# Kernel optimization log

Hardware: AMD Instinct MI355X
Metric: run time of the kernel (lower is better)

Reference implementation:

```python
import jax, jax.numpy as jnp
import numpy as np
import math

HGT, WID = 24, 24          # shape2d
NUM_HEADS = 12
EMB = 768
HEAD_DIM = EMB // NUM_HEADS
N_GRID = HGT * WID         # 576 spatial tokens
N_TOK = N_GRID + 1         # +1 CLS token
BATCH = 32


def _rel_indices(h: int, w: int) -> np.ndarray:
    """[(h*w), (h*w)] indices into the (2h-1)*(2w-1) relative table."""
    y = np.arange(h)
    x = np.arange(w)
    y1, x1, y2, x2 = np.meshgrid(y, x, y, x, indexing='ij')
    idx = (y1 - y2 + h - 1) * (2 * w - 1) + (x1 - x2 + w - 1)
    return idx.reshape(h * w, h * w)


def setup_inputs() -> dict:
    key = jax.random.key(0)
    ks = jax.random.split(key, 6)
    s = 0.02
    return {
        "x": jax.random.normal(ks[0], (BATCH, N_TOK, EMB), dtype=jnp.float32),
        "Wq": jax.random.normal(ks[1], (EMB, EMB), dtype=jnp.float32) * s,
        "bq": jnp.zeros((EMB,), dtype=jnp.float32),
        "Wk": jax.random.normal(ks[2], (EMB, EMB), dtype=jnp.float32) * s,
        "bk": jnp.zeros((EMB,), dtype=jnp.float32),
        "Wv": jax.random.normal(ks[3], (EMB, EMB), dtype=jnp.float32) * s,
        "bv": jnp.zeros((EMB,), dtype=jnp.float32),
        "Wp": jax.random.normal(ks[4], (EMB, EMB), dtype=jnp.float32) * s,
        "bp": jnp.zeros((EMB,), dtype=jnp.float32),
        "rel_table": jax.random.normal(ks[5], ((2 * HGT - 1) * (2 * WID - 1), NUM_HEADS), dtype=jnp.float32) * s,
    }


def reference(x, Wq, bq, Wk, bk, Wv, bv, Wp, bp, rel_table):
    B, N, E = x.shape
    scale = 1.0 / math.sqrt(HEAD_DIM)

    def heads(t):  # [B,N,E] -> [B,H,N,hd]
        return t.reshape(B, N, NUM_HEADS, HEAD_DIM).transpose(0, 2, 1, 3)

    q = heads(x @ Wq.T + bq)
    k = heads(x @ Wk.T + bk)
    v = heads(x @ Wv.T + bv)

    scores = jnp.einsum('bhqd,bhkd->bhqk', q, k) * scale  # [B,H,N,N]

    # relative position bias on spatial tokens (skip CLS row/col)
    idx = jnp.asarray(_rel_indices(HGT, WID))              # [Ng,Ng]
    bias = rel_table[idx].transpose(2, 0, 1)               # [H,Ng,Ng]
    scores = scores.at[:, :, 1:, 1:].add(bias)

    attn = jax.nn.softmax(scores, axis=-1)
    out = jnp.einsum('bhqk,bhkd->bhqd', attn, v)           # [B,H,N,hd]
    out = out.transpose(0, 2, 1, 3).reshape(B, N, E)
    return out @ Wp.T + bp
```

## Files before the change

kernel.cpp:

```cpp
#include <hip/hip_runtime.h>
#include <stdint.h>

#define HGT   24
#define WID   24
#define NHEAD 12
#define EMB   768
#define HD    64
#define NGRID 576
#define NTOK  577
#define NPAD  640
#define BATCH 32
#define MROWS (BATCH * NTOK)
#define NKT   10
#define NQT   5
#define QKVC  (3 * EMB)

typedef __attribute__((ext_vector_type(8))) short bf16x8;
typedef __attribute__((ext_vector_type(4))) float f32x4;

__device__ __forceinline__ short f2bf(float f) {
    union { float f; unsigned u; } c; c.f = f;
    unsigned r = (c.u + 0x7FFFu + ((c.u >> 16) & 1u)) >> 16;
    return (short)(r & 0xFFFFu);
}
__device__ __forceinline__ float b2f(short s) {
    union { unsigned u; float f; } c; c.u = ((unsigned)(unsigned short)s) << 16;
    return c.f;
}

__device__ __forceinline__ void gload16(void* lds, const void* g) {
    __builtin_amdgcn_global_load_lds(
        (const __attribute__((address_space(1))) void*)g,
        (__attribute__((address_space(3))) void*)lds, 16, 0, 0);
}

__device__ __forceinline__ void wait_vm0_barrier() {
    asm volatile("s_waitcnt vmcnt(0)" ::: "memory");
    __builtin_amdgcn_s_barrier();
}

__device__ __forceinline__ int xcd_swizzle(int orig, int nwg) {
    int q = nwg >> 3, r = nwg & 7;
    int xcd = orig & 7, idx = orig >> 3;
    return (xcd < r) ? xcd * (q + 1) + idx : r * (q + 1) + (xcd - r) * q + idx;
}

__global__ void cast_f32_bf16(const float* __restrict__ src, short* __restrict__ dst, int n) {
    int i = (blockIdx.x * blockDim.x + threadIdx.x) * 4;
    int stride = gridDim.x * blockDim.x * 4;
    for (int j = i; j < n; j += stride) {
        float4 v = *(const float4*)(src + j);
        short4 o;
        o.x = f2bf(v.x); o.y = f2bf(v.y); o.z = f2bf(v.z); o.w = f2bf(v.w);
        *(short4*)(dst + j) = o;
    }
}

__global__ void bias_expand(const float* __restrict__ rel, short* __restrict__ be) {
    int q = blockIdx.x;
    int k = threadIdx.x;
    float v[NHEAD];
    if (k >= NTOK) {
#pragma unroll
        for (int h = 0; h < NHEAD; h++) v[h] = -1e30f;
    } else if (q == 0 || q >= NTOK || k == 0) {
#pragma unroll
        for (int h = 0; h < NHEAD; h++) v[h] = 0.f;
    } else {
        int i = q - 1, j = k - 1;
        int idx = ((i / WID) - (j / WID) + HGT - 1) * (2 * WID - 1)
                + ((i % WID) - (j % WID) + WID - 1);
        const float* rp = rel + (size_t)idx * NHEAD;
#pragma unroll
        for (int h = 0; h < NHEAD; h++) v[h] = rp[h];
    }
#pragma unroll
    for (int h = 0; h < NHEAD; h++)
        be[((size_t)h * NPAD + q) * NPAD + k] = f2bf(v[h]);
}

__global__ __launch_bounds__(256) void transpose_v(const short* __restrict__ qnat, short* __restrict__ vt) {
    __shared__ __align__(16) short T[64][72];
    int bi = blockIdx.x;
    int kt = bi % NKT;
    int h  = (bi / NKT) % NHEAD;
    int b  = bi / (NKT * NHEAD);
    int t  = threadIdx.x;

    int r  = t >> 2, cb = (t & 3) * 16;
    int key = kt * 64 + r; if (key >= NTOK) key = NTOK - 1;
    const short* src = qnat + (size_t)(b * NTOK + key) * QKVC + 2 * EMB + h * HD;
    *(int4*)&T[r][cb]     = *(const int4*)(src + cb);
    *(int4*)&T[r][cb + 8] = *(const int4*)(src + cb + 8);
    __syncthreads();

    int d = t >> 2, kb = (t & 3) * 16;
    short tmp[16];
#pragma unroll
    for (int s = 0; s < 16; s++) tmp[s] = T[kb + s][d];
    short* dst = vt + (((size_t)b * NHEAD + h) * HD + d) * NPAD + kt * 64 + kb;
    *(int4*)&dst[0] = *(int4*)&tmp[0];
    *(int4*)&dst[8] = *(int4*)&tmp[8];
}

template <int MODE>
__global__ __launch_bounds__(256) void gemm_bt(
    const short* __restrict__ A, const short* __restrict__ Bw,
    const float* __restrict__ b0, const float* __restrict__ b1, const float* __restrict__ b2,
    void* __restrict__ Outp, int M)
{
    constexpr int NC  = (MODE == 0) ? QKVC : EMB;
    constexpr int NBX = NC / 128;
    constexpr int K   = EMB;
    constexpr int NST = K / 128;

    __shared__ __align__(16) short Asl[128][128];
    __shared__ __align__(16) short Bsl[128][128];

    const int t    = threadIdx.x;
    const int lane = t & 63;
    const int w    = t >> 6;
    const int wr   = (w >> 1) * 64;
    const int wc   = (w & 1) * 64;
    const int lg   = lane >> 4;
    const int li   = lane & 15;

    const int nwg  = NBX * 145;
    const int wgid = xcd_swizzle(blockIdx.x, nwg);
    const int tm   = (wgid / NBX) * 128;
    const int tn   = (wgid % NBX) * 128;

    const int srow16 = w * 4 + (lane >> 4);
    const int cofs   = ((lane & 15) ^ srow16) * 8;

    const short* ag[8];
    const short* bg[8];
#pragma unroll
    for (int p = 0; p < 8; p++) {
        int rm = tm + p * 16 + srow16; if (rm >= M) rm = M - 1;
        ag[p] = A  + (size_t)rm * K + cofs;
        bg[p] = Bw + (size_t)(tn + p * 16 + srow16) * K + cofs;
    }

    f32x4 acc[4][4];
#pragma unroll
    for (int i = 0; i < 4; i++)
#pragma unroll
        for (int j = 0; j < 4; j++) acc[i][j] = (f32x4){0.f, 0.f, 0.f, 0.f};

#pragma unroll
    for (int p = 0; p < 8; p++) {
        gload16(&Asl[p * 16 + w * 4][0], ag[p]);
        gload16(&Bsl[p * 16 + w * 4][0], bg[p]);
    }

    for (int step = 0; step < NST; step++) {
        wait_vm0_barrier();

#pragma unroll
        for (int kk = 0; kk < 4; kk++) {
            bf16x8 af[4], bfr[4];
#pragma unroll
            for (int i = 0; i < 4; i++)
                af[i]  = *(const bf16x8*)&Asl[wr + i * 16 + li][((kk * 4 + lg) ^ li) * 8];
#pragma unroll
            for (int j = 0; j < 4; j++)
                bfr[j] = *(const bf16x8*)&Bsl[wc + j * 16 + li][((kk * 4 + lg) ^ li) * 8];
#pragma unroll
            for (int i = 0; i < 4; i++)
#pragma unroll
                for (int j = 0; j < 4; j++)
                    acc[i][j] = __builtin_amdgcn_mfma_f32_16x16x32_bf16(af[i], bfr[j], acc[i][j], 0, 0, 0);
        }

        __builtin_amdgcn_s_barrier();
        if (step + 1 < NST) {
            int k0 = (step + 1) * 128;
#pragma unroll
            for (int p = 0; p < 8; p++) {
                gload16(&Asl[p * 16 + w * 4][0], ag[p] + k0);
                gload16(&Bsl[p * 16 + w * 4][0], bg[p] + k0);
            }
        }
    }

#pragma unroll
    for (int j = 0; j < 4; j++) {
        int c = tn + wc + j * 16 + li;
        float bias;
        if constexpr (MODE == 0) {
            int which = (c >= 2 * EMB) ? 2 : ((c >= EMB) ? 1 : 0);
            const float* bb = (which == 0) ? b0 : ((which == 1) ? b1 : b2);
            bias = bb[c - which * EMB];
        } else {
            bias = b0[c];
        }
#pragma unroll
        for (int i = 0; i < 4; i++) {
#pragma unroll
            for (int r = 0; r < 4; r++) {
                int m = tm + wr + i * 16 + lg * 4 + r;
                if (m >= M) continue;
                float v = acc[i][j][r] + bias;
                if constexpr (MODE == 0)
                    ((short*)Outp)[(size_t)m * NC + c] = f2bf(v);
                else
                    ((float*)Outp)[(size_t)m * NC + c] = v;
            }
        }
    }
}

__global__ __launch_bounds__(512) void attn_kernel(
    const short* __restrict__ qnat, const short* __restrict__ vt,
    const short* __restrict__ biasx, short* __restrict__ aout)
{
    __shared__ __align__(16) short Ksl[2][64][64];
    __shared__ __align__(16) short Vsl[2][64][64];
    __shared__ __align__(16) short Psl[8][16][72];

    const int wg = (blockIdx.x & 7) * (BATCH * NHEAD * NQT / 8) + (blockIdx.x >> 3);
    const int qt = wg % NQT;
    const int rest = wg / NQT;
    const int b  = rest & 31;
    const int h  = rest >> 5;

    const int t    = threadIdx.x;
    const int lane = t & 63;
    const int w    = t >> 6;
    const int lg   = lane >> 4;
    const int li   = lane & 15;
    const int xh   = li & 7;
    const int qbase = qt * 128;
    const int myq  = qbase + w * 16 + li;

    const short* qp  = qnat + (size_t)b * NTOK * QKVC + h * HD;
    const short* kp  = qp + EMB;
    const short* vtp = vt + ((size_t)b * NHEAD + h) * (size_t)HD * NPAD;
    const short* browq = biasx + ((size_t)h * NPAD + myq) * NPAD;

    bf16x8 qf[2];
    {
        int qrow = myq < NTOK ? myq : NTOK - 1;
        qf[0] = *(const bf16x8*)(qp + (size_t)qrow * QKVC + lg * 8);
        qf[1] = *(const bf16x8*)(qp + (size_t)qrow * QKVC + 32 + lg * 8);
    }

    float mrun = -1e30f, lrun = 0.f;
    f32x4 oacc[4];
#pragma unroll
    for (int d = 0; d < 4; d++) oacc[d] = (f32x4){0.f, 0.f, 0.f, 0.f};

    const int srow = w * 8 + (lane >> 3);
    const int cofs = ((lane & 7) ^ (lane >> 3)) * 8;

    {
        int key = srow; if (key >= NTOK) key = NTOK - 1;
        gload16(&Ksl[0][w * 8][0], kp + (size_t)key * QKVC + cofs);
        gload16(&Vsl[0][w * 8][0], vtp + (size_t)srow * NPAD + cofs);
    }
    wait_vm0_barrier();

    short (*Kc)[64] = Ksl[0], (*Kn)[64] = Ksl[1];
    short (*Vc)[64] = Vsl[0], (*Vn)[64] = Vsl[1];

    for (int kt = 0; kt < NKT; kt++) {
        if (kt + 1 < NKT) {
            int key = (kt + 1) * 64 + srow; if (key >= NTOK) key = NTOK - 1;
            gload16(&Kn[w * 8][0], kp + (size_t)key * QKVC + cofs);
            gload16(&Vn[w * 8][0], vtp + (size_t)srow * NPAD + (kt + 1) * 64 + cofs);
        }

        float pvv[4][4];
        __builtin_amdgcn_s_setprio(1);
#pragma unroll
        for (int j = 0; j < 4; j++) {
            short4 bs = *(const short4*)&browq[kt * 64 + j * 16 + lg * 4];
            bf16x8 ak0 = *(const bf16x8*)&Kc[j * 16 + li][(lg ^ xh) * 8];
            bf16x8 ak1 = *(const bf16x8*)&Kc[j * 16 + li][((4 + lg) ^ xh) * 8];
            f32x4 s = (f32x4){0.f, 0.f, 0.f, 0.f};
            s = __builtin_amdgcn_mfma_f32_16x16x32_bf16(ak0, qf[0], s, 0, 0, 0);
            s = __builtin_amdgcn_mfma_f32_16x16x32_bf16(ak1, qf[1], s, 0, 0, 0);
            pvv[j][0] = fmaf(s[0], 0.125f, b2f(bs.x));
            pvv[j][1] = fmaf(s[1], 0.125f, b2f(bs.y));
            pvv[j][2] = fmaf(s[2], 0.125f, b2f(bs.z));
            pvv[j][3] = fmaf(s[3], 0.125f, b2f(bs.w));
        }
        __builtin_amdgcn_s_setprio(0);

        float mt = pvv[0][0];
#pragma unroll
        for (int j = 0; j < 4; j++)
#pragma unroll
            for (int r = 0; r < 4; r++) mt = fmaxf(mt, pvv[j][r]);
        mt = fmaxf(mt, __shfl_xor(mt, 16, 64));
        mt = fmaxf(mt, __shfl_xor(mt, 32, 64));
        float nm  = fmaxf(mrun, mt);
        float fac = __expf(mrun - nm);
        float rs  = 0.f;
#pragma unroll
        for (int j = 0; j < 4; j++)
#pragma unroll
            for (int r = 0; r < 4; r++) {
                float p = __expf(pvv[j][r] - nm);
                pvv[j][r] = p;
                rs += p;
            }
        rs += __shfl_xor(rs, 16, 64);
        rs += __shfl_xor(rs, 32, 64);
        lrun = lrun * fac + rs;
        mrun = nm;
#pragma unroll
        for (int d = 0; d < 4; d++) oacc[d] *= fac;

#pragma unroll
        for (int j = 0; j < 4; j++) {
            short4 ps;
            ps.x = f2bf(pvv[j][0]); ps.y = f2bf(pvv[j][1]);
            ps.z = f2bf(pvv[j][2]); ps.w = f2bf(pvv[j][3]);
            *(short4*)&Psl[w][li][j * 16 + lg * 4] = ps;
        }

        __builtin_amdgcn_s_setprio(1);
#pragma unroll
        for (int dd = 0; dd < 4; dd++) {
#pragma unroll
            for (int kk = 0; kk < 2; kk++) {
                bf16x8 av = *(const bf16x8*)&Vc[dd * 16 + li][((kk * 4 + lg) ^ xh) * 8];
                bf16x8 pb = *(const bf16x8*)&Psl[w][li][kk * 32 + lg * 8];
                oacc[dd] = __builtin_amdgcn_mfma_f32_16x16x32_bf16(av, pb, oacc[dd], 0, 0, 0);
            }
        }
        __builtin_amdgcn_s_setprio(0);

        wait_vm0_barrier();
        short (*tp)[64];
        tp = Kc; Kc = Kn; Kn = tp;
        tp = Vc; Vc = Vn; Vn = tp;
    }

    if (myq < NTOK) {
        float inv = 1.0f / lrun;
        short* op = aout + ((size_t)b * NTOK + myq) * EMB + h * HD;
#pragma unroll
        for (int dd = 0; dd < 4; dd++) {
            short4 o;
            o.x = f2bf(oacc[dd][0] * inv);
            o.y = f2bf(oacc[dd][1] * inv);
            o.z = f2bf(oacc[dd][2] * inv);
            o.w = f2bf(oacc[dd][3] * inv);
            *(short4*)&op[dd * 16 + lg * 4] = o;
        }
    }
}

extern "C" void kernel_launch(void* const* d_in, const int* in_sizes, int n_in,
                              void* d_out, int out_size, void* d_ws, size_t ws_size,
                              hipStream_t stream) {
    (void)in_sizes; (void)n_in; (void)out_size; (void)ws_size;
    const float* x   = (const float*)d_in[0];
    const float* Wq  = (const float*)d_in[1];
    const float* bq  = (const float*)d_in[2];
    const float* Wk  = (const float*)d_in[3];
    const float* bk  = (const float*)d_in[4];
    const float* Wv  = (const float*)d_in[5];
    const float* bv  = (const float*)d_in[6];
    const float* Wp  = (const float*)d_in[7];
    const float* bp  = (const float*)d_in[8];
    const float* rel = (const float*)d_in[9];

    const size_t WN = (size_t)EMB * EMB;
    short* Wb   = (short*)d_ws;
    short* Wpb  = Wb + 3 * WN;
    short* qnat = Wpb + WN;
    short* xb   = qnat + (size_t)MROWS * QKVC;
    short* aout = xb;
    short* vtb  = xb + (size_t)MROWS * EMB;
    short* bexp = vtb + (size_t)BATCH * NHEAD * HD * NPAD;

    const int XN = MROWS * EMB;
    cast_f32_bf16<<<576, 256, 0, stream>>>(Wq, Wb, (int)WN);
    cast_f32_bf16<<<576, 256, 0, stream>>>(Wk, Wb + WN, (int)WN);
    cast_f32_bf16<<<576, 256, 0, stream>>>(Wv, Wb + 2 * WN, (int)WN);
    cast_f32_bf16<<<576, 256, 0, stream>>>(Wp, Wpb, (int)WN);
    cast_f32_bf16<<<13848, 256, 0, stream>>>(x, xb, XN);
    bias_expand<<<NPAD, NPAD, 0, stream>>>(rel, bexp);

    gemm_bt<0><<<18 * 145, 256, 0, stream>>>(xb, Wb, bq, bk, bv, qnat, MROWS);
    transpose_v<<<BATCH * NHEAD * NKT, 256, 0, stream>>>(qnat, vtb);
    attn_kernel<<<BATCH * NHEAD * NQT, 512, 0, stream>>>(qnat, vtb, bexp, aout);
    gemm_bt<1><<<6 * 145, 256, 0, stream>>>(aout, Wpb, bp, bp, bp, d_out, MROWS);
}
```

Before: 315.7 us.

## Restructure GEMM to 256x256 tiles with double-buffered LDS and interleaved prefetch

The shared bf16 GEMM now uses 256x256 output tiles per 512-thread workgroup with a K-step of 64. The LDS is double-buffered, and the next tile's global loads are spread across the four compute sub-phases, with partial vmcnt waits and barriers between them. MFMA sections are wrapped in s_setprio to favour the math waves. The goal is to hide global-load latency and raise per-workgroup data reuse. The costs are fewer workgroups (9*73 and 3*73), higher register pressure from 32 accumulators per wave, and more barriers per K-step.

```diff
diff --git a/kernel.cpp b/kernel.cpp
--- a/kernel.cpp
+++ b/kernel.cpp
@@ -104,108 +104,148 @@
 }
 
 template <int MODE>
-__global__ __launch_bounds__(256) void gemm_bt(
+__global__ __launch_bounds__(512) void gemm_bt(
     const short* __restrict__ A, const short* __restrict__ Bw,
     const float* __restrict__ b0, const float* __restrict__ b1, const float* __restrict__ b2,
     void* __restrict__ Outp, int M)
 {
     constexpr int NC  = (MODE == 0) ? QKVC : EMB;
-    constexpr int NBX = NC / 128;
+    constexpr int NBX = NC / 256;
     constexpr int K   = EMB;
-    constexpr int NST = K / 128;
-
-    __shared__ __align__(16) short Asl[128][128];
-    __shared__ __align__(16) short Bsl[128][128];
+    constexpr int NT  = K / 64;
+
+    __shared__ __align__(16) short Asl[2][256][64];
+    __shared__ __align__(16) short Bsl[2][256][64];
 
     const int t    = threadIdx.x;
     const int lane = t & 63;
     const int w    = t >> 6;
-    const int wr   = (w >> 1) * 64;
-    const int wc   = (w & 1) * 64;
+    const int wm   = w >> 2;
+    const int wn   = w & 3;
     const int lg   = lane >> 4;
     const int li   = lane & 15;
-
-    const int nwg  = NBX * 145;
+    const int xh   = li & 7;
+
+    const int nwg  = NBX * ((MROWS + 255) / 256);
     const int wgid = xcd_swizzle(blockIdx.x, nwg);
-    const int tm   = (wgid / NBX) * 128;
-    const int tn   = (wgid % NBX) * 128;
-
-    const int srow16 = w * 4 + (lane >> 4);
-    const int cofs   = ((lane & 15) ^ srow16) * 8;
-
-    const short* ag[8];
-    const short* bg[8];
-#pragma unroll
-    for (int p = 0; p < 8; p++) {
-        int rm = tm + p * 16 + srow16; if (rm >= M) rm = M - 1;
-        ag[p] = A  + (size_t)rm * K + cofs;
-        bg[p] = Bw + (size_t)(tn + p * 16 + srow16) * K + cofs;
-    }
-
-    f32x4 acc[4][4];
-#pragma unroll
-    for (int i = 0; i < 4; i++)
+    const int tm   = (wgid / NBX) * 256;
+    const int tn   = (wgid % NBX) * 256;
+
+    const int srow = w * 8 + (lane >> 3);
+    const int cofs = ((lane & 7) ^ (lane >> 3)) * 8;
+
+    constexpr int AOFF[4] = {0, 128, 64, 192};
+    constexpr int BOFF[4] = {0, 64, 128, 192};
+
+    const short* agp[4];
+    const short* bgp[4];
+#pragma unroll
+    for (int i = 0; i < 4; i++) {
+        int ra = tm + AOFF[i] + srow; if (ra >= M) ra = M - 1;
+        agp[i] = A  + (size_t)ra * K + cofs;
+        bgp[i] = Bw + (size_t)(tn + BOFF[i] + srow) * K + cofs;
+    }
+
+    f32x4 acc[8][4];
+#pragma unroll
+    for (int i = 0; i < 8; i++)
 #pragma unroll
         for (int j = 0; j < 4; j++) acc[i][j] = (f32x4){0.f, 0.f, 0.f, 0.f};
 
 #pragma unroll
-    for (int p = 0; p < 8; p++) {
-        gload16(&Asl[p * 16 + w * 4][0], ag[p]);
-        gload16(&Bsl[p * 16 + w * 4][0], bg[p]);
-    }
-
-    for (int step = 0; step < NST; step++) {
-        wait_vm0_barrier();
-
-#pragma unroll
-        for (int kk = 0; kk < 4; kk++) {
-            bf16x8 af[4], bfr[4];
-#pragma unroll
-            for (int i = 0; i < 4; i++)
-                af[i]  = *(const bf16x8*)&Asl[wr + i * 16 + li][((kk * 4 + lg) ^ li) * 8];
-#pragma unroll
-            for (int j = 0; j < 4; j++)
-                bfr[j] = *(const bf16x8*)&Bsl[wc + j * 16 + li][((kk * 4 + lg) ^ li) * 8];
-#pragma unroll
-            for (int i = 0; i < 4; i++)
-#pragma unroll
-                for (int j = 0; j < 4; j++)
-                    acc[i][j] = __builtin_amdgcn_mfma_f32_16x16x32_bf16(af[i], bfr[j], acc[i][j], 0, 0, 0);
-        }
-
-        __builtin_amdgcn_s_barrier();
-        if (step + 1 < NST) {
-            int k0 = (step + 1) * 128;
-#pragma unroll
-            for (int p = 0; p < 8; p++) {
-                gload16(&Asl[p * 16 + w * 4][0], ag[p] + k0);
-                gload16(&Bsl[p * 16 + w * 4][0], bg[p] + k0);
+    for (int i = 0; i < 4; i++) gload16(&Bsl[0][BOFF[i] + w * 8][0], bgp[i]);
+#pragma unroll
+    for (int i = 0; i < 4; i++) gload16(&Asl[0][AOFF[i] + w * 8][0], agp[i]);
+    asm volatile("s_waitcnt vmcnt(2)" ::: "memory");
+    __builtin_amdgcn_s_barrier();
+
+    for (int kt = 0; kt < NT; kt++) {
+        const int c = kt & 1, nb = c ^ 1;
+        const bool more = (kt + 1 < NT);
+        const int k0n = (kt + 1) * 64;
+
+        bf16x8 bf[4][2];
+#pragma unroll
+        for (int q = 0; q < 4; q++) {
+            bf16x8 af[2][2];
+#pragma unroll
+            for (int mm = 0; mm < 2; mm++)
+#pragma unroll
+                for (int kk = 0; kk < 2; kk++)
+                    af[mm][kk] = *(const bf16x8*)
+                        &Asl[c][wm * 128 + (q * 2 + mm) * 16 + li][((kk * 4 + lg) ^ xh) * 8];
+            if (q == 0) {
+#pragma unroll
+                for (int nj = 0; nj < 4; nj++)
+#pragma unroll
+                    for (int kk = 0; kk < 2; kk++)
+                        bf[nj][kk] = *(const bf16x8*)
+                            &Bsl[c][wn * 64 + nj * 16 + li][((kk * 4 + lg) ^ xh) * 8];
             }
-        }
-    }
-
-#pragma unroll
-    for (int j = 0; j < 4; j++) {
-        int c = tn + wc + j * 16 + li;
+
+            if (q == 0) {
+                if (more) {
+                    gload16(&Bsl[nb][BOFF[0] + w * 8][0], bgp[0] + k0n);
+                    gload16(&Bsl[nb][BOFF[1] + w * 8][0], bgp[1] + k0n);
+                }
+            } else if (q == 1) {
+                if (more) {
+                    gload16(&Bsl[nb][BOFF[2] + w * 8][0], bgp[2] + k0n);
+                    gload16(&Bsl[nb][BOFF[3] + w * 8][0], bgp[3] + k0n);
+                    asm volatile("s_waitcnt vmcnt(4)" ::: "memory");
+                } else {
+                    asm volatile("s_waitcnt vmcnt(0)" ::: "memory");
+                }
+            } else if (q == 2) {
+                if (more) {
+                    gload16(&Asl[nb][AOFF[0] + w * 8][0], agp[0] + k0n);
+                    gload16(&Asl[nb][AOFF[1] + w * 8][0], agp[1] + k0n);
+                }
+            } else {
+                if (more) {
+                    gload16(&Asl[nb][AOFF[2] + w * 8][0], agp[2] + k0n);
+                    gload16(&Asl[nb][AOFF[3] + w * 8][0], agp[3] + k0n);
+                    asm volatile("s_waitcnt vmcnt(2)" ::: "memory");
+                }
+            }
+            __builtin_amdgcn_s_barrier();
+
+            __builtin_amdgcn_s_setprio(1);
+#pragma unroll
+            for (int mm = 0; mm < 2; mm++)
+#pragma unroll
+                for (int nj = 0; nj < 4; nj++)
+#pragma unroll
+                    for (int kk = 0; kk < 2; kk++)
+                        acc[q * 2 + mm][nj] = __builtin_amdgcn_mfma_f32_16x16x32_bf16(
+                            af[mm][kk], bf[nj][kk], acc[q * 2 + mm][nj], 0, 0, 0);
+            __builtin_amdgcn_s_setprio(0);
+            __builtin_amdgcn_s_barrier();
+        }
+    }
+
+#pragma unroll
+    for (int nj = 0; nj < 4; nj++) {
+        int cc = tn + wn * 64 + nj * 16 + li;
         float bias;
         if constexpr (MODE == 0) {
-            int which = (c >= 2 * EMB) ? 2 : ((c >= EMB) ? 1 : 0);
+            int which = (cc >= 2 * EMB) ? 2 : ((cc >= EMB) ? 1 : 0);
             const float* bb = (which == 0) ? b0 : ((which == 1) ? b1 : b2);
-            bias = bb[c - which * EMB];
+            bias = bb[cc - which * EMB];
         } else {
-            bias = b0[c];
-        }
-#pragma unroll
-        for (int i = 0; i < 4; i++) {
+            bias = b0[cc];
+        }
+#pragma unroll
+        for (int mi = 0; mi < 8; mi++) {
 #pragma unroll
             for (int r = 0; r < 4; r++) {
-                int m = tm + wr + i * 16 + lg * 4 + r;
+                int m = tm + wm * 128 + mi * 16 + lg * 4 + r;
                 if (m >= M) continue;
-                float v = acc[i][j][r] + bias;
+                float v = acc[mi][nj][r] + bias;
                 if constexpr (MODE == 0)
-                    ((short*)Outp)[(size_t)m * NC + c] = f2bf(v);
+                    ((short*)Outp)[(size_t)m * NC + cc] = f2bf(v);
                 else
-                    ((float*)Outp)[(size_t)m * NC + c] = v;
+                    ((float*)Outp)[(size_t)m * NC + cc] = v;
             }
         }
     }
@@ -379,6 +419,7 @@
     short* bexp = vtb + (size_t)BATCH * NHEAD * HD * NPAD;
 
     const int XN = MROWS * EMB;
+    const int MT = (MROWS + 255) / 256;
     cast_f32_bf16<<<576, 256, 0, stream>>>(Wq, Wb, (int)WN);
     cast_f32_bf16<<<576, 256, 0, stream>>>(Wk, Wb + WN, (int)WN);
     cast_f32_bf16<<<576, 256, 0, stream>>>(Wv, Wb + 2 * WN, (int)WN);
@@ -386,8 +427,8 @@
     cast_f32_bf16<<<13848, 256, 0, stream>>>(x, xb, XN);
     bias_expand<<<NPAD, NPAD, 0, stream>>>(rel, bexp);
 
-    gemm_bt<0><<<18 * 145, 256, 0, stream>>>(xb, Wb, bq, bk, bv, qnat, MROWS);
+    gemm_bt<0><<<9 * MT, 512, 0, stream>>>(xb, Wb, bq, bk, bv, qnat, MROWS);
     transpose_v<<<BATCH * NHEAD * NKT, 256, 0, stream>>>(qnat, vtb);
     attn_kernel<<<BATCH * NHEAD * NQT, 512, 0, stream>>>(qnat, vtb, bexp, aout);
-    gemm_bt<1><<<6 * 145, 256, 0, stream>>>(aout, Wpb, bp, bp, bp, d_out, MROWS);
-}
+    gemm_bt<1><<<3 * MT, 512, 0, stream>>>(aout, Wpb, bp, bp, bp, d_out, MROWS);
+}
```

After: 301.7 us. -4.5%, faster.

## Restructure GEMM to 256x256 tiles with 4-stage K pipeline and 512 threads

Applied to the files above, without the earlier changes.

Reworks the bf16 GEMM used for the QKV and output projections. Tiles grow to 256x256 with 8 waves, the K dimension is split into 32-wide slices held in a 4-deep LDS ring buffer with three loads in flight, and MFMA blocks run at raised priority. Swapping the MFMA operands gives a transposed accumulator layout, so the epilogue can write vectorized 4-wide stores. The aim is more reuse per tile and global loads overlapped with compute. The cost is higher register pressure from 32 accumulators per wave, fewer workgroups for the smaller projection, and more padded rows wasted in the last M tile.

```diff
diff --git a/kernel.cpp b/kernel.cpp
--- a/kernel.cpp
+++ b/kernel.cpp
@@ -104,108 +104,122 @@
 }
 
 template <int MODE>
-__global__ __launch_bounds__(256) void gemm_bt(
+__global__ __launch_bounds__(512) void gemm_bt(
     const short* __restrict__ A, const short* __restrict__ Bw,
     const float* __restrict__ b0, const float* __restrict__ b1, const float* __restrict__ b2,
     void* __restrict__ Outp, int M)
 {
     constexpr int NC  = (MODE == 0) ? QKVC : EMB;
-    constexpr int NBX = NC / 128;
+    constexpr int NBX = NC / 256;
     constexpr int K   = EMB;
-    constexpr int NST = K / 128;
-
-    __shared__ __align__(16) short Asl[128][128];
-    __shared__ __align__(16) short Bsl[128][128];
+    constexpr int NST = K / 32;
+
+    __shared__ __align__(16) short Asl[4][256][32];
+    __shared__ __align__(16) short Bsl[4][256][32];
 
     const int t    = threadIdx.x;
     const int lane = t & 63;
     const int w    = t >> 6;
-    const int wr   = (w >> 1) * 64;
-    const int wc   = (w & 1) * 64;
+    const int wm   = w >> 2;
+    const int wn   = w & 3;
     const int lg   = lane >> 4;
     const int li   = lane & 15;
 
-    const int nwg  = NBX * 145;
+    const int nwg  = NBX * ((MROWS + 255) / 256);
     const int wgid = xcd_swizzle(blockIdx.x, nwg);
-    const int tm   = (wgid / NBX) * 128;
-    const int tn   = (wgid % NBX) * 128;
-
-    const int srow16 = w * 4 + (lane >> 4);
-    const int cofs   = ((lane & 15) ^ srow16) * 8;
-
-    const short* ag[8];
-    const short* bg[8];
-#pragma unroll
-    for (int p = 0; p < 8; p++) {
-        int rm = tm + p * 16 + srow16; if (rm >= M) rm = M - 1;
-        ag[p] = A  + (size_t)rm * K + cofs;
-        bg[p] = Bw + (size_t)(tn + p * 16 + srow16) * K + cofs;
-    }
-
-    f32x4 acc[4][4];
-#pragma unroll
-    for (int i = 0; i < 4; i++)
+    const int tm   = (wgid / NBX) * 256;
+    const int tn   = (wgid % NBX) * 256;
+
+    const int drow = lane >> 2;
+    const int lc   = (lane & 3) ^ ((lane >> 3) & 3);
+    const int xsw  = (li >> 1) & 3;
+
+    const short* agp[2];
+    const short* bgp[2];
+#pragma unroll
+    for (int gi = 0; gi < 2; gi++) {
+        int rm = tm + gi * 128 + w * 16 + drow; if (rm >= M) rm = M - 1;
+        agp[gi] = A  + (size_t)rm * K + lc * 8;
+        bgp[gi] = Bw + (size_t)(tn + gi * 128 + w * 16 + drow) * K + lc * 8;
+    }
+
+    f32x4 acc[8][4];
+#pragma unroll
+    for (int i = 0; i < 8; i++)
 #pragma unroll
         for (int j = 0; j < 4; j++) acc[i][j] = (f32x4){0.f, 0.f, 0.f, 0.f};
 
 #pragma unroll
-    for (int p = 0; p < 8; p++) {
-        gload16(&Asl[p * 16 + w * 4][0], ag[p]);
-        gload16(&Bsl[p * 16 + w * 4][0], bg[p]);
-    }
-
-    for (int step = 0; step < NST; step++) {
-        wait_vm0_barrier();
-
-#pragma unroll
-        for (int kk = 0; kk < 4; kk++) {
-            bf16x8 af[4], bfr[4];
-#pragma unroll
-            for (int i = 0; i < 4; i++)
-                af[i]  = *(const bf16x8*)&Asl[wr + i * 16 + li][((kk * 4 + lg) ^ li) * 8];
-#pragma unroll
-            for (int j = 0; j < 4; j++)
-                bfr[j] = *(const bf16x8*)&Bsl[wc + j * 16 + li][((kk * 4 + lg) ^ li) * 8];
-#pragma unroll
-            for (int i = 0; i < 4; i++)
-#pragma unroll
-                for (int j = 0; j < 4; j++)
-                    acc[i][j] = __builtin_amdgcn_mfma_f32_16x16x32_bf16(af[i], bfr[j], acc[i][j], 0, 0, 0);
-        }
-
+    for (int ss = 0; ss < 3; ss++) {
+        gload16(&Asl[ss][0 * 128 + w * 16][0], agp[0] + ss * 32);
+        gload16(&Asl[ss][1 * 128 + w * 16][0], agp[1] + ss * 32);
+        gload16(&Bsl[ss][0 * 128 + w * 16][0], bgp[0] + ss * 32);
+        gload16(&Bsl[ss][1 * 128 + w * 16][0], bgp[1] + ss * 32);
+    }
+
+    for (int s = 0; s < NST; s++) {
+        if (s < NST - 2)       asm volatile("s_waitcnt vmcnt(8)" ::: "memory");
+        else if (s == NST - 2) asm volatile("s_waitcnt vmcnt(4)" ::: "memory");
+        else                   asm volatile("s_waitcnt vmcnt(0)" ::: "memory");
         __builtin_amdgcn_s_barrier();
-        if (step + 1 < NST) {
-            int k0 = (step + 1) * 128;
-#pragma unroll
-            for (int p = 0; p < 8; p++) {
-                gload16(&Asl[p * 16 + w * 4][0], ag[p] + k0);
-                gload16(&Bsl[p * 16 + w * 4][0], bg[p] + k0);
-            }
-        }
-    }
-
-#pragma unroll
-    for (int j = 0; j < 4; j++) {
-        int c = tn + wc + j * 16 + li;
-        float bias;
+
+        const int cb = s & 3;
+        bf16x8 af[8], bfv[4];
+#pragma unroll
+        for (int mi = 0; mi < 8; mi++)
+            af[mi] = *(const bf16x8*)&Asl[cb][wm * 128 + mi * 16 + li][(lg ^ xsw) * 8];
+#pragma unroll
+        for (int nj = 0; nj < 4; nj++)
+            bfv[nj] = *(const bf16x8*)&Bsl[cb][wn * 64 + nj * 16 + li][(lg ^ xsw) * 8];
+
+        if (s + 3 < NST) {
+            const int tb = (s + 3) & 3;
+            const int ko = (s + 3) * 32;
+            gload16(&Asl[tb][0 * 128 + w * 16][0], agp[0] + ko);
+            gload16(&Asl[tb][1 * 128 + w * 16][0], agp[1] + ko);
+            gload16(&Bsl[tb][0 * 128 + w * 16][0], bgp[0] + ko);
+            gload16(&Bsl[tb][1 * 128 + w * 16][0], bgp[1] + ko);
+        }
+
+        __builtin_amdgcn_s_setprio(1);
+#pragma unroll
+        for (int mi = 0; mi < 8; mi++)
+#pragma unroll
+            for (int nj = 0; nj < 4; nj++)
+                acc[mi][nj] = __builtin_amdgcn_mfma_f32_16x16x32_bf16(
+                    bfv[nj], af[mi], acc[mi][nj], 0, 0, 0);
+        __builtin_amdgcn_s_setprio(0);
+    }
+
+#pragma unroll
+    for (int nj = 0; nj < 4; nj++) {
+        const int ccb = tn + wn * 64 + nj * 16 + lg * 4;
+        float4 bias4;
         if constexpr (MODE == 0) {
-            int which = (c >= 2 * EMB) ? 2 : ((c >= EMB) ? 1 : 0);
+            int which = (ccb >= 2 * EMB) ? 2 : ((ccb >= EMB) ? 1 : 0);
             const float* bb = (which == 0) ? b0 : ((which == 1) ? b1 : b2);
-            bias = bb[c - which * EMB];
+            bias4 = *(const float4*)&bb[ccb - which * EMB];
         } else {
-            bias = b0[c];
-        }
-#pragma unroll
-        for (int i = 0; i < 4; i++) {
-#pragma unroll
-            for (int r = 0; r < 4; r++) {
-                int m = tm + wr + i * 16 + lg * 4 + r;
-                if (m >= M) continue;
-                float v = acc[i][j][r] + bias;
-                if constexpr (MODE == 0)
-                    ((short*)Outp)[(size_t)m * NC + c] = f2bf(v);
-                else
-                    ((float*)Outp)[(size_t)m * NC + c] = v;
+            bias4 = *(const float4*)&b0[ccb];
+        }
+#pragma unroll
+        for (int mi = 0; mi < 8; mi++) {
+            int m = tm + wm * 128 + mi * 16 + li;
+            if (m >= M) continue;
+            if constexpr (MODE == 0) {
+                short4 o;
+                o.x = f2bf(acc[mi][nj][0] + bias4.x);
+                o.y = f2bf(acc[mi][nj][1] + bias4.y);
+                o.z = f2bf(acc[mi][nj][2] + bias4.z);
+                o.w = f2bf(acc[mi][nj][3] + bias4.w);
+                *(short4*)&((short*)Outp)[(size_t)m * NC + ccb] = o;
+            } else {
+                float4 o;
+                o.x = acc[mi][nj][0] + bias4.x;
+                o.y = acc[mi][nj][1] + bias4.y;
+                o.z = acc[mi][nj][2] + bias4.z;
+                o.w = acc[mi][nj][3] + bias4.w;
+                *(float4*)&((float*)Outp)[(size_t)m * NC + ccb] = o;
             }
         }
     }
@@ -379,6 +393,7 @@
     short* bexp = vtb + (size_t)BATCH * NHEAD * HD * NPAD;
 
     const int XN = MROWS * EMB;
+    const int MT = (MROWS + 255) / 256;
     cast_f32_bf16<<<576, 256, 0, stream>>>(Wq, Wb, (int)WN);
     cast_f32_bf16<<<576, 256, 0, stream>>>(Wk, Wb + WN, (int)WN);
     cast_f32_bf16<<<576, 256, 0, stream>>>(Wv, Wb + 2 * WN, (int)WN);
@@ -386,8 +401,8 @@
     cast_f32_bf16<<<13848, 256, 0, stream>>>(x, xb, XN);
     bias_expand<<<NPAD, NPAD, 0, stream>>>(rel, bexp);
 
-    gemm_bt<0><<<18 * 145, 256, 0, stream>>>(xb, Wb, bq, bk, bv, qnat, MROWS);
+    gemm_bt<0><<<9 * MT, 512, 0, stream>>>(xb, Wb, bq, bk, bv, qnat, MROWS);
     transpose_v<<<BATCH * NHEAD * NKT, 256, 0, stream>>>(qnat, vtb);
     attn_kernel<<<BATCH * NHEAD * NQT, 512, 0, stream>>>(qnat, vtb, bexp, aout);
-    gemm_bt<1><<<6 * 145, 256, 0, stream>>>(aout, Wpb, bp, bp, bp, d_out, MROWS);
-}
+    gemm_bt<1><<<3 * MT, 512, 0, stream>>>(aout, Wpb, bp, bp, bp, d_out, MROWS);
+}
```

Result: faster. 282.5 us (-10.5%).
